# Optimization experiments

Hardware: AMD Instinct MI355X
Metric: run time of the kernel (lower is better)

The kernel has to match this reference:

```python
import jax, jax.numpy as jnp
import numpy as np

N_NODES = 50000
N_EDGES = 500000
D_IN = 128
D_HID = 128
OUTPUT_DIM = 10.0


def gcn_conv(x, src, dst, edge_weight, W, b, n_nodes):
    # PyG GCNConv: out = D^{-1/2} (A + I) D^{-1/2} X W + b, self-loop weight 1
    xw = x @ W  # [N, D_out]
    # degree at target nodes, including self-loop weight 1
    deg = jax.ops.segment_sum(edge_weight, dst, num_segments=n_nodes) + 1.0
    dinv = jnp.where(deg > 0, jax.lax.rsqrt(deg), 0.0)  # [N]
    norm = dinv[src] * edge_weight * dinv[dst]  # [E]
    msgs = xw[src] * norm[:, None]  # [E, D_out] gathered+scaled messages
    agg = jax.ops.segment_sum(msgs, dst, num_segments=n_nodes)
    # analytic self-loop contribution: norm_ii = dinv_i * 1 * dinv_i
    agg = agg + xw * (dinv * dinv)[:, None]
    return agg + b


def setup_inputs() -> dict:
    key = jax.random.key(0)
    k = jax.random.split(key, 8)
    x = jax.random.normal(k[0], (N_NODES, D_IN), dtype=jnp.float32)
    edge_index = jax.random.randint(k[1], (2, N_EDGES), 0, N_NODES, dtype=jnp.int64)
    edge_weight = jax.random.uniform(k[2], (N_EDGES,), dtype=jnp.float32)
    s1 = 1.0 / np.sqrt(D_IN)
    s2 = 1.0 / np.sqrt(D_HID)
    W1 = jax.random.uniform(k[3], (D_IN, D_HID), minval=-s1, maxval=s1, dtype=jnp.float32)
    b1 = jnp.zeros((D_HID,), dtype=jnp.float32)
    W2 = jax.random.uniform(k[4], (D_HID, D_HID), minval=-s2, maxval=s2, dtype=jnp.float32)
    b2 = jnp.zeros((D_HID,), dtype=jnp.float32)
    Wf = jax.random.uniform(k[5], (D_HID, 1), minval=-s2, maxval=s2, dtype=jnp.float32)
    bf = jax.random.uniform(k[6], (1,), minval=-s2, maxval=s2, dtype=jnp.float32)
    return {"x": x, "edge_index": edge_index, "edge_weight": edge_weight,
            "W1": W1, "b1": b1, "W2": W2, "b2": b2, "Wf": Wf, "bf": bf}


def reference(x, edge_index, edge_weight, W1, b1, W2, b2, Wf, bf):
    src, dst = edge_index[0], edge_index[1]
    h = gcn_conv(x, src, dst, edge_weight, W1, b1, N_NODES)
    h = gcn_conv(h, src, dst, edge_weight, W2, b2, N_NODES)
    out = h @ Wf + bf  # [N, 1]
    return jax.nn.sigmoid(out) * OUTPUT_DIM
```

## Files before the change

### kernel.cpp

```cpp
#include <hip/hip_runtime.h>

#define N_NODES 50000
#define N_EDGES 500000
#define D 128
#define CAP 64
#define NCHUNK 256
#define EPC ((N_EDGES + NCHUNK - 1) / NCHUNK)
#define NWORDS ((N_NODES + 3) / 4)

typedef unsigned long long u64;

__global__ void hist_kernel(const int* __restrict__ dst,
                            const float* __restrict__ W1, const float* __restrict__ W2,
                            const float* __restrict__ b1, const float* __restrict__ b2,
                            const float* __restrict__ Wf, const float* __restrict__ bf,
                            unsigned* __restrict__ hist32, float* __restrict__ v,
                            float* __restrict__ consts) {
    if ((int)blockIdx.x == NCHUNK) {
        __shared__ float u[D];
        int t = threadIdx.x;
        if (t < D) {
            float a = 0.f;
#pragma unroll 8
            for (int j = 0; j < D; ++j) a += W2[t * D + j] * Wf[j];
            u[t] = a;
        }
        __syncthreads();
        if (t < D) {
            float a = 0.f;
#pragma unroll 8
            for (int k = 0; k < D; ++k) a += W1[t * D + k] * u[k];
            v[t] = a;
        }
        if (t == 0) {
            float c = 0.f;
            for (int k = 0; k < D; ++k) c += b1[k] * u[k];
            consts[0] = c;
        } else if (t == 1) {
            float c = bf[0];
            for (int k = 0; k < D; ++k) c += b2[k] * Wf[k];
            consts[1] = c;
        }
        return;
    }
    __shared__ unsigned lds[NWORDS];
    const int t = threadIdx.x;
    const int c = blockIdx.x;
    for (int i = t; i < NWORDS; i += 256) lds[i] = 0u;
    __syncthreads();
    const int e0 = c * EPC;
    const int e1 = (e0 + EPC < N_EDGES) ? e0 + EPC : N_EDGES;
    for (int e = e0 + t; e < e1; e += 256) {
        int d = dst[e];
        atomicAdd(&lds[d >> 2], 1u << (8 * (d & 3)));
    }
    __syncthreads();
    unsigned* outw = hist32 + (size_t)c * NWORDS;
    for (int i = t; i < NWORDS; i += 256) outw[i] = lds[i];
}

__global__ void scan_kernel(const unsigned char* __restrict__ hist8,
                            unsigned char* __restrict__ base8, int* __restrict__ cntv) {
    int n = blockIdx.x * blockDim.x + threadIdx.x;
    if (n >= N_NODES) return;
    int run = 0;
#pragma unroll 8
    for (int c = 0; c < NCHUNK; ++c) {
        int b = hist8[(size_t)c * (NWORDS * 4) + n];
        base8[(size_t)c * (NWORDS * 4) + n] = (unsigned char)run;
        run += b;
    }
    cntv[n] = (run < CAP) ? run : CAP;
}

__global__ void place_kernel(const int* __restrict__ src, const int* __restrict__ dst,
                             const float* __restrict__ ew,
                             const unsigned* __restrict__ base32, int2* __restrict__ pairs) {
    __shared__ unsigned lds[NWORDS];
    const int t = threadIdx.x;
    const int c = blockIdx.x;
    const unsigned* inw = base32 + (size_t)c * NWORDS;
    for (int i = t; i < NWORDS; i += 256) lds[i] = inw[i];
    __syncthreads();
    const int e0 = c * EPC;
    const int e1 = (e0 + EPC < N_EDGES) ? e0 + EPC : N_EDGES;
    for (int e = e0 + t; e < e1; e += 256) {
        int d = dst[e];
        int sh = 8 * (d & 3);
        unsigned old = atomicAdd(&lds[d >> 2], 1u << sh);
        int slot = (int)((old >> sh) & 0xffu);
        if (slot < CAP)
            pairs[(size_t)d * CAP + slot] = make_int2(src[e], __float_as_int(ew[e]));
    }
}

__global__ void gemv_kernel(const float* __restrict__ x, const float* __restrict__ v,
                            const int2* __restrict__ pairs, const int* __restrict__ cntv,
                            float* __restrict__ dinv, float* __restrict__ tw) {
    __shared__ float vs[D];
    const int t = threadIdx.x;
    if (t < D) vs[t] = v[t];
    __syncthreads();
    const int l = t & 31;
    const int n = blockIdx.x * 8 + (t >> 5);
    float4 xv = ((const float4*)(x + (size_t)n * D))[l];
    float a = xv.x * vs[l * 4] + xv.y * vs[l * 4 + 1] +
              xv.z * vs[l * 4 + 2] + xv.w * vs[l * 4 + 3];
    int cnt = cntv[n];
    const int2* row = pairs + (size_t)n * CAP;
    float wsum = 0.f;
    for (int i = l; i < cnt; i += 32) wsum += __int_as_float(row[i].y);
#pragma unroll
    for (int off = 16; off > 0; off >>= 1) {
        a    += __shfl_xor(a, off);
        wsum += __shfl_xor(wsum, off);
    }
    if (l == 0) {
        float di = rsqrtf(wsum + 1.0f);
        dinv[n] = di;
        tw[n] = di * a;
    }
}

__global__ void gather_s_kernel(const float* __restrict__ tw, const float* __restrict__ dinv,
                                const int* __restrict__ cntv, const int2* __restrict__ pairs,
                                const float* __restrict__ consts, float* __restrict__ sw) {
    int tid = threadIdx.x;
    int n = blockIdx.x * 64 + (tid >> 2);
    int l = tid & 3;
    if (n >= N_NODES) return;
    int cnt = cntv[n];
    const int4* row = (const int4*)(pairs + (size_t)n * CAP);
    float acc = 0.f;
    for (int c = l; 2 * c < cnt; c += 4) {
        int4 p = row[c];
        acc += __int_as_float(p.y) * tw[p.x];
        if (2 * c + 1 < cnt) acc += __int_as_float(p.w) * tw[p.z];
    }
    acc += __shfl_xor(acc, 1);
    acc += __shfl_xor(acc, 2);
    if (l == 0) {
        float di = dinv[n];
        float s = di * (acc + tw[n]) + consts[0];
        sw[n] = di * s;
    }
}

__global__ void gather_z_kernel(const float* __restrict__ sw, const float* __restrict__ dinv,
                                const int* __restrict__ cntv, const int2* __restrict__ pairs,
                                const float* __restrict__ consts, float* __restrict__ out) {
    int tid = threadIdx.x;
    int n = blockIdx.x * 64 + (tid >> 2);
    int l = tid & 3;
    if (n >= N_NODES) return;
    int cnt = cntv[n];
    const int4* row = (const int4*)(pairs + (size_t)n * CAP);
    float acc = 0.f;
    for (int c = l; 2 * c < cnt; c += 4) {
        int4 p = row[c];
        acc += __int_as_float(p.y) * sw[p.x];
        if (2 * c + 1 < cnt) acc += __int_as_float(p.w) * sw[p.z];
    }
    acc += __shfl_xor(acc, 1);
    acc += __shfl_xor(acc, 2);
    if (l == 0) {
        float di = dinv[n];
        float z = di * (acc + sw[n]) + consts[1];
        out[n] = 10.0f / (1.0f + expf(-z));
    }
}

extern "C" void kernel_launch(void* const* d_in, const int* in_sizes, int n_in,
                              void* d_out, int out_size, void* d_ws, size_t ws_size,
                              hipStream_t stream) {
    const float* x  = (const float*)d_in[0];
    const int*   ei = (const int*)d_in[1];
    const float* ew = (const float*)d_in[2];
    const float* W1 = (const float*)d_in[3];
    const float* b1 = (const float*)d_in[4];
    const float* W2 = (const float*)d_in[5];
    const float* b2 = (const float*)d_in[6];
    const float* Wf = (const float*)d_in[7];
    const float* bf = (const float*)d_in[8];
    const int* srcv = ei;
    const int* dstv = ei + N_EDGES;
    float* out = (float*)d_out;

    char* p = (char*)d_ws;
    auto alloc = [&](size_t bytes) { void* r = (void*)p; p += (bytes + 255) & ~(size_t)255; return r; };
    unsigned*      hist32 = (unsigned*)alloc((size_t)NCHUNK * NWORDS * 4);
    unsigned char* base8  = (unsigned char*)alloc((size_t)NCHUNK * NWORDS * 4);
    int*   cntv   = (int*)alloc(N_NODES * 4);
    float* dinv   = (float*)alloc(N_NODES * 4);
    float* tw     = (float*)alloc(N_NODES * 4);
    float* sw     = (float*)alloc(N_NODES * 4);
    float* v      = (float*)alloc(D * 4);
    float* consts = (float*)alloc(2 * 4);
    int2*  pairs  = (int2*)alloc((size_t)N_NODES * CAP * 8);

    const int GB = (N_NODES + 63) / 64;
    const int NB = (N_NODES + 255) / 256;

    hist_kernel<<<NCHUNK + 1, 256, 0, stream>>>(dstv, W1, W2, b1, b2, Wf, bf,
                                                hist32, v, consts);

    scan_kernel<<<NB, 256, 0, stream>>>((const unsigned char*)hist32, base8, cntv);

    place_kernel<<<NCHUNK, 256, 0, stream>>>(srcv, dstv, ew,
                                             (const unsigned*)base8, pairs);

    gemv_kernel<<<N_NODES / 8, 256, 0, stream>>>(x, v, pairs, cntv, dinv, tw);

    gather_s_kernel<<<GB, 256, 0, stream>>>(tw, dinv, cntv, pairs, consts, sw);
    gather_z_kernel<<<GB, 256, 0, stream>>>(sw, dinv, cntv, pairs, consts, out);
}
```

Measured before the change: 140.8 us.

## Rewrite chunk scan as packed-word LDS scan across chunk partitions

Replaces the per-node serial byte scan over 256 chunks with a block-level scan operating on packed 32-bit words (four byte counters each), splitting the chunk dimension across four thread groups with an LDS carry combine. Reads and writes become 32-bit coalesced instead of byte-wide strided, and cntv is written as int4. Relies on byte counters not overflowing into neighbours, which the original byte layout already assumed. Uses 64KB+ of LDS per block, which limits occupancy.

```diff
diff --git a/kernel.cpp b/kernel.cpp
--- a/kernel.cpp
+++ b/kernel.cpp
@@ -5,10 +5,10 @@
 #define D 128
 #define CAP 64
 #define NCHUNK 256
-#define EPC ((N_EDGES + NCHUNK - 1) / NCHUNK)
-#define NWORDS ((N_NODES + 3) / 4)
-
-typedef unsigned long long u64;
+#define EPC 1954
+#define NWORDS 12500
+#define SCAN_W 64
+#define SCAN_BLOCKS ((NWORDS + SCAN_W - 1) / SCAN_W)
 
 __global__ void hist_kernel(const int* __restrict__ dst,
                             const float* __restrict__ W1, const float* __restrict__ W2,
@@ -59,18 +59,51 @@
     for (int i = t; i < NWORDS; i += 256) outw[i] = lds[i];
 }
 
-__global__ void scan_kernel(const unsigned char* __restrict__ hist8,
-                            unsigned char* __restrict__ base8, int* __restrict__ cntv) {
-    int n = blockIdx.x * blockDim.x + threadIdx.x;
-    if (n >= N_NODES) return;
-    int run = 0;
-#pragma unroll 8
-    for (int c = 0; c < NCHUNK; ++c) {
-        int b = hist8[(size_t)c * (NWORDS * 4) + n];
-        base8[(size_t)c * (NWORDS * 4) + n] = (unsigned char)run;
-        run += b;
-    }
-    cntv[n] = (run < CAP) ? run : CAP;
+__global__ __launch_bounds__(256) void scan_kernel(const unsigned* __restrict__ hist32,
+                                                   unsigned* __restrict__ base32,
+                                                   int* __restrict__ cntv) {
+    __shared__ unsigned lds[NCHUNK][SCAN_W];
+    __shared__ unsigned tot[4][SCAN_W];
+    const int t = threadIdx.x;
+    const int cp = t >> 6;
+    const int w = t & 63;
+    const int gw = blockIdx.x * SCAN_W + w;
+    const bool valid = gw < NWORDS;
+    for (int cc = 0; cc < 64; ++cc) {
+        int c = cp * 64 + cc;
+        lds[c][w] = valid ? hist32[(size_t)c * NWORDS + gw] : 0u;
+    }
+    __syncthreads();
+    unsigned run = 0u;
+    for (int cc = 0; cc < 64; ++cc) {
+        int c = cp * 64 + cc;
+        unsigned x = lds[c][w];
+        lds[c][w] = run;
+        run += x;
+    }
+    tot[cp][w] = run;
+    __syncthreads();
+    unsigned off = 0u;
+    for (int j = 0; j < cp; ++j) off += tot[j][w];
+    for (int cc = 0; cc < 64; ++cc) {
+        int c = cp * 64 + cc;
+        lds[c][w] += off;
+    }
+    if (cp == 0 && valid) {
+        unsigned tl = tot[0][w] + tot[1][w] + tot[2][w] + tot[3][w];
+        int4 cv;
+        cv.x = min((int)(tl & 0xffu), CAP);
+        cv.y = min((int)((tl >> 8) & 0xffu), CAP);
+        cv.z = min((int)((tl >> 16) & 0xffu), CAP);
+        cv.w = min((int)((tl >> 24) & 0xffu), CAP);
+        ((int4*)cntv)[gw] = cv;
+    }
+    if (valid) {
+        for (int cc = 0; cc < 64; ++cc) {
+            int c = cp * 64 + cc;
+            base32[(size_t)c * NWORDS + gw] = lds[c][w];
+        }
+    }
 }
 
 __global__ void place_kernel(const int* __restrict__ src, const int* __restrict__ dst,
@@ -188,8 +221,8 @@
 
     char* p = (char*)d_ws;
     auto alloc = [&](size_t bytes) { void* r = (void*)p; p += (bytes + 255) & ~(size_t)255; return r; };
-    unsigned*      hist32 = (unsigned*)alloc((size_t)NCHUNK * NWORDS * 4);
-    unsigned char* base8  = (unsigned char*)alloc((size_t)NCHUNK * NWORDS * 4);
+    unsigned* hist32 = (unsigned*)alloc((size_t)NCHUNK * NWORDS * 4);
+    unsigned* base32 = (unsigned*)alloc((size_t)NCHUNK * NWORDS * 4);
     int*   cntv   = (int*)alloc(N_NODES * 4);
     float* dinv   = (float*)alloc(N_NODES * 4);
     float* tw     = (float*)alloc(N_NODES * 4);
@@ -199,15 +232,11 @@
     int2*  pairs  = (int2*)alloc((size_t)N_NODES * CAP * 8);
 
     const int GB = (N_NODES + 63) / 64;
-    const int NB = (N_NODES + 255) / 256;
 
     hist_kernel<<<NCHUNK + 1, 256, 0, stream>>>(dstv, W1, W2, b1, b2, Wf, bf,
                                                 hist32, v, consts);
-
-    scan_kernel<<<NB, 256, 0, stream>>>((const unsigned char*)hist32, base8, cntv);
-
-    place_kernel<<<NCHUNK, 256, 0, stream>>>(srcv, dstv, ew,
-                                             (const unsigned*)base8, pairs);
+    scan_kernel<<<SCAN_BLOCKS, 256, 0, stream>>>(hist32, base32, cntv);
+    place_kernel<<<NCHUNK, 256, 0, stream>>>(srcv, dstv, ew, base32, pairs);
 
     gemv_kernel<<<N_NODES / 8, 256, 0, stream>>>(x, v, pairs, cntv, dinv, tw);
 
```

Result: slower. 149.4 us (+6.1%).

## Replace per-chunk byte histograms with two-level bucketed CSR construction

Applied to the files above, without the earlier changes.

Replaces the 256-chunk LDS byte histogram, per-node serial scan and placement into fixed 64-slot rows with a two-pass bucket sort. The first pass scatters edge records into 98 coarse destination buckets through global atomic allocation. The second pass builds a compact CSR per 512-node bucket with an LDS count, a scan and placement, and rows are padded to even length for int4 reads. This removes the large hist/base arrays and the sparse padded pair layout, in exchange for an extra record write and read. Correctness relies on each bucket holding at most 8192 edges, which holds for uniform random inputs.

```diff
diff --git a/kernel.cpp b/kernel.cpp
--- a/kernel.cpp
+++ b/kernel.cpp
@@ -2,100 +2,132 @@
 
 #define N_NODES 50000
 #define N_EDGES 500000
+#define NQ (N_EDGES / 4)
 #define D 128
 #define CAP 64
-#define NCHUNK 256
-#define EPC ((N_EDGES + NCHUNK - 1) / NCHUNK)
-#define NWORDS ((N_NODES + 3) / 4)
-
-typedef unsigned long long u64;
-
-__global__ void hist_kernel(const int* __restrict__ dst,
-                            const float* __restrict__ W1, const float* __restrict__ W2,
+#define NBUCK 98
+#define BN 512
+#define REG 8192
+
+__global__ void prep_kernel(const float* __restrict__ W1, const float* __restrict__ W2,
                             const float* __restrict__ b1, const float* __restrict__ b2,
                             const float* __restrict__ Wf, const float* __restrict__ bf,
-                            unsigned* __restrict__ hist32, float* __restrict__ v,
-                            float* __restrict__ consts) {
-    if ((int)blockIdx.x == NCHUNK) {
-        __shared__ float u[D];
-        int t = threadIdx.x;
-        if (t < D) {
-            float a = 0.f;
+                            float* __restrict__ v, float* __restrict__ consts,
+                            unsigned* __restrict__ alloc) {
+    const int t = threadIdx.x;
+    if (blockIdx.x == 1) {
+        if (t < 128) alloc[t] = 0u;
+        return;
+    }
+    __shared__ float u[D];
+    if (t < D) {
+        float a = 0.f;
 #pragma unroll 8
-            for (int j = 0; j < D; ++j) a += W2[t * D + j] * Wf[j];
-            u[t] = a;
-        }
+        for (int j = 0; j < D; ++j) a += W2[t * D + j] * Wf[j];
+        u[t] = a;
+    }
+    __syncthreads();
+    if (t < D) {
+        float a = 0.f;
+#pragma unroll 8
+        for (int k = 0; k < D; ++k) a += W1[t * D + k] * u[k];
+        v[t] = a;
+    }
+    if (t == 0) {
+        float c = 0.f;
+        for (int k = 0; k < D; ++k) c += b1[k] * u[k];
+        consts[0] = c;
+    } else if (t == 1) {
+        float c = bf[0];
+        for (int k = 0; k < D; ++k) c += b2[k] * Wf[k];
+        consts[1] = c;
+    }
+}
+
+__global__ void bucket_kernel(const int* __restrict__ src, const int* __restrict__ dst,
+                              const float* __restrict__ ew,
+                              unsigned* __restrict__ alloc, unsigned* __restrict__ recs) {
+    __shared__ unsigned hist[NBUCK];
+    const int t = threadIdx.x;
+    if (t < NBUCK) hist[t] = 0u;
+    __syncthreads();
+    const int q = blockIdx.x * 256 + t;
+    const bool act = q < NQ;
+    int4 d4 = make_int4(0, 0, 0, 0), s4 = make_int4(0, 0, 0, 0);
+    float4 w4 = make_float4(0.f, 0.f, 0.f, 0.f);
+    int b0 = 0, b1 = 0, b2 = 0, b3 = 0;
+    if (act) {
+        d4 = ((const int4*)dst)[q];
+        s4 = ((const int4*)src)[q];
+        w4 = ((const float4*)ew)[q];
+        b0 = d4.x >> 9; b1 = d4.y >> 9; b2 = d4.z >> 9; b3 = d4.w >> 9;
+        atomicAdd(&hist[b0], 1u); atomicAdd(&hist[b1], 1u);
+        atomicAdd(&hist[b2], 1u); atomicAdd(&hist[b3], 1u);
+    }
+    __syncthreads();
+    if (t < NBUCK) hist[t] = atomicAdd(&alloc[t], hist[t]);
+    __syncthreads();
+    if (act) {
+        unsigned p;
+        p = atomicAdd(&hist[b0], 1u);
+        if (p < REG) { size_t o = ((size_t)b0 * REG + p) * 3;
+            recs[o] = (unsigned)d4.x; recs[o+1] = (unsigned)s4.x; recs[o+2] = __float_as_uint(w4.x); }
+        p = atomicAdd(&hist[b1], 1u);
+        if (p < REG) { size_t o = ((size_t)b1 * REG + p) * 3;
+            recs[o] = (unsigned)d4.y; recs[o+1] = (unsigned)s4.y; recs[o+2] = __float_as_uint(w4.y); }
+        p = atomicAdd(&hist[b2], 1u);
+        if (p < REG) { size_t o = ((size_t)b2 * REG + p) * 3;
+            recs[o] = (unsigned)d4.z; recs[o+1] = (unsigned)s4.z; recs[o+2] = __float_as_uint(w4.z); }
+        p = atomicAdd(&hist[b3], 1u);
+        if (p < REG) { size_t o = ((size_t)b3 * REG + p) * 3;
+            recs[o] = (unsigned)d4.w; recs[o+1] = (unsigned)s4.w; recs[o+2] = __float_as_uint(w4.w); }
+    }
+}
+
+__global__ __launch_bounds__(512) void csr_kernel(const unsigned* __restrict__ recs,
+                                                  const unsigned* __restrict__ alloc,
+                                                  int2* __restrict__ csr,
+                                                  unsigned* __restrict__ rowptr,
+                                                  int* __restrict__ cntv) {
+    __shared__ unsigned cnt[BN], pfx[BN], cur[BN];
+    const int b = blockIdx.x, t = threadIdx.x;
+    const int nb0 = b * BN;
+    const int nnode = (N_NODES - nb0 < BN) ? (N_NODES - nb0) : BN;
+    unsigned total = alloc[b];
+    if (total > REG) total = REG;
+    cnt[t] = 0u;
+    __syncthreads();
+    const unsigned* rb = recs + (size_t)b * REG * 3;
+    for (unsigned i = t; i < total; i += 512)
+        atomicAdd(&cnt[rb[i * 3] - nb0], 1u);
+    __syncthreads();
+    const unsigned c = cnt[t];
+    const unsigned cR = (c + 1u) & ~1u;
+    pfx[t] = cR;
+    __syncthreads();
+    for (int off = 1; off < BN; off <<= 1) {
+        unsigned vv = (t >= off) ? pfx[t - off] : 0u;
         __syncthreads();
-        if (t < D) {
-            float a = 0.f;
-#pragma unroll 8
-            for (int k = 0; k < D; ++k) a += W1[t * D + k] * u[k];
-            v[t] = a;
-        }
-        if (t == 0) {
-            float c = 0.f;
-            for (int k = 0; k < D; ++k) c += b1[k] * u[k];
-            consts[0] = c;
-        } else if (t == 1) {
-            float c = bf[0];
-            for (int k = 0; k < D; ++k) c += b2[k] * Wf[k];
-            consts[1] = c;
-        }
-        return;
-    }
-    __shared__ unsigned lds[NWORDS];
-    const int t = threadIdx.x;
-    const int c = blockIdx.x;
-    for (int i = t; i < NWORDS; i += 256) lds[i] = 0u;
-    __syncthreads();
-    const int e0 = c * EPC;
-    const int e1 = (e0 + EPC < N_EDGES) ? e0 + EPC : N_EDGES;
-    for (int e = e0 + t; e < e1; e += 256) {
-        int d = dst[e];
-        atomicAdd(&lds[d >> 2], 1u << (8 * (d & 3)));
-    }
-    __syncthreads();
-    unsigned* outw = hist32 + (size_t)c * NWORDS;
-    for (int i = t; i < NWORDS; i += 256) outw[i] = lds[i];
-}
-
-__global__ void scan_kernel(const unsigned char* __restrict__ hist8,
-                            unsigned char* __restrict__ base8, int* __restrict__ cntv) {
-    int n = blockIdx.x * blockDim.x + threadIdx.x;
-    if (n >= N_NODES) return;
-    int run = 0;
-#pragma unroll 8
-    for (int c = 0; c < NCHUNK; ++c) {
-        int b = hist8[(size_t)c * (NWORDS * 4) + n];
-        base8[(size_t)c * (NWORDS * 4) + n] = (unsigned char)run;
-        run += b;
-    }
-    cntv[n] = (run < CAP) ? run : CAP;
-}
-
-__global__ void place_kernel(const int* __restrict__ src, const int* __restrict__ dst,
-                             const float* __restrict__ ew,
-                             const unsigned* __restrict__ base32, int2* __restrict__ pairs) {
-    __shared__ unsigned lds[NWORDS];
-    const int t = threadIdx.x;
-    const int c = blockIdx.x;
-    const unsigned* inw = base32 + (size_t)c * NWORDS;
-    for (int i = t; i < NWORDS; i += 256) lds[i] = inw[i];
-    __syncthreads();
-    const int e0 = c * EPC;
-    const int e1 = (e0 + EPC < N_EDGES) ? e0 + EPC : N_EDGES;
-    for (int e = e0 + t; e < e1; e += 256) {
-        int d = dst[e];
-        int sh = 8 * (d & 3);
-        unsigned old = atomicAdd(&lds[d >> 2], 1u << sh);
-        int slot = (int)((old >> sh) & 0xffu);
-        if (slot < CAP)
-            pairs[(size_t)d * CAP + slot] = make_int2(src[e], __float_as_int(ew[e]));
+        pfx[t] += vv;
+        __syncthreads();
+    }
+    const unsigned excl = pfx[t] - cR;
+    cur[t] = excl;
+    if (t < nnode) {
+        rowptr[nb0 + t] = (unsigned)(b * REG) + excl;
+        cntv[nb0 + t] = (c < CAP) ? (int)c : CAP;
+    }
+    __syncthreads();
+    for (unsigned i = t; i < total; i += 512) {
+        unsigned d = rb[i * 3], s = rb[i * 3 + 1], w = rb[i * 3 + 2];
+        unsigned r = atomicAdd(&cur[d - nb0], 1u);
+        csr[(size_t)b * REG + r] = make_int2((int)s, (int)w);
     }
 }
 
 __global__ void gemv_kernel(const float* __restrict__ x, const float* __restrict__ v,
-                            const int2* __restrict__ pairs, const int* __restrict__ cntv,
+                            const int2* __restrict__ csr, const unsigned* __restrict__ rowptr,
+                            const int* __restrict__ cntv,
                             float* __restrict__ dinv, float* __restrict__ tw) {
     __shared__ float vs[D];
     const int t = threadIdx.x;
@@ -107,7 +139,7 @@
     float a = xv.x * vs[l * 4] + xv.y * vs[l * 4 + 1] +
               xv.z * vs[l * 4 + 2] + xv.w * vs[l * 4 + 3];
     int cnt = cntv[n];
-    const int2* row = pairs + (size_t)n * CAP;
+    const int2* row = csr + rowptr[n];
     float wsum = 0.f;
     for (int i = l; i < cnt; i += 32) wsum += __int_as_float(row[i].y);
 #pragma unroll
@@ -123,14 +155,15 @@
 }
 
 __global__ void gather_s_kernel(const float* __restrict__ tw, const float* __restrict__ dinv,
-                                const int* __restrict__ cntv, const int2* __restrict__ pairs,
+                                const int* __restrict__ cntv, const int2* __restrict__ csr,
+                                const unsigned* __restrict__ rowptr,
                                 const float* __restrict__ consts, float* __restrict__ sw) {
     int tid = threadIdx.x;
     int n = blockIdx.x * 64 + (tid >> 2);
     int l = tid & 3;
     if (n >= N_NODES) return;
     int cnt = cntv[n];
-    const int4* row = (const int4*)(pairs + (size_t)n * CAP);
+    const int4* row = (const int4*)(csr + rowptr[n]);
     float acc = 0.f;
     for (int c = l; 2 * c < cnt; c += 4) {
         int4 p = row[c];
@@ -147,14 +180,15 @@
 }
 
 __global__ void gather_z_kernel(const float* __restrict__ sw, const float* __restrict__ dinv,
-                                const int* __restrict__ cntv, const int2* __restrict__ pairs,
+                                const int* __restrict__ cntv, const int2* __restrict__ csr,
+                                const unsigned* __restrict__ rowptr,
                                 const float* __restrict__ consts, float* __restrict__ out) {
     int tid = threadIdx.x;
     int n = blockIdx.x * 64 + (tid >> 2);
     int l = tid & 3;
     if (n >= N_NODES) return;
     int cnt = cntv[n];
-    const int4* row = (const int4*)(pairs + (size_t)n * CAP);
+    const int4* row = (const int4*)(csr + rowptr[n]);
     float acc = 0.f;
     for (int c = l; 2 * c < cnt; c += 4) {
         int4 p = row[c];
@@ -187,30 +221,28 @@
     float* out = (float*)d_out;
 
     char* p = (char*)d_ws;
-    auto alloc = [&](size_t bytes) { void* r = (void*)p; p += (bytes + 255) & ~(size_t)255; return r; };
-    unsigned*      hist32 = (unsigned*)alloc((size_t)NCHUNK * NWORDS * 4);
-    unsigned char* base8  = (unsigned char*)alloc((size_t)NCHUNK * NWORDS * 4);
-    int*   cntv   = (int*)alloc(N_NODES * 4);
-    float* dinv   = (float*)alloc(N_NODES * 4);
-    float* tw     = (float*)alloc(N_NODES * 4);
-    float* sw     = (float*)alloc(N_NODES * 4);
-    float* v      = (float*)alloc(D * 4);
-    float* consts = (float*)alloc(2 * 4);
-    int2*  pairs  = (int2*)alloc((size_t)N_NODES * CAP * 8);
-
+    auto alloc_ws = [&](size_t bytes) { void* r = (void*)p; p += (bytes + 255) & ~(size_t)255; return r; };
+    unsigned* alloc  = (unsigned*)alloc_ws(128 * 4);
+    unsigned* recs   = (unsigned*)alloc_ws((size_t)NBUCK * REG * 12);
+    int2*     csr    = (int2*)alloc_ws((size_t)NBUCK * REG * 8);
+    unsigned* rowptr = (unsigned*)alloc_ws(N_NODES * 4);
+    int*      cntv   = (int*)alloc_ws(N_NODES * 4);
+    float*    dinv   = (float*)alloc_ws(N_NODES * 4);
+    float*    tw     = (float*)alloc_ws(N_NODES * 4);
+    float*    sw     = (float*)alloc_ws(N_NODES * 4);
+    float*    v      = (float*)alloc_ws(D * 4);
+    float*    consts = (float*)alloc_ws(2 * 4);
+
+    const int AB = (NQ + 255) / 256;
     const int GB = (N_NODES + 63) / 64;
-    const int NB = (N_NODES + 255) / 256;
-
-    hist_kernel<<<NCHUNK + 1, 256, 0, stream>>>(dstv, W1, W2, b1, b2, Wf, bf,
-                                                hist32, v, consts);
-
-    scan_kernel<<<NB, 256, 0, stream>>>((const unsigned char*)hist32, base8, cntv);
-
-    place_kernel<<<NCHUNK, 256, 0, stream>>>(srcv, dstv, ew,
-                                             (const unsigned*)base8, pairs);
-
-    gemv_kernel<<<N_NODES / 8, 256, 0, stream>>>(x, v, pairs, cntv, dinv, tw);
-
-    gather_s_kernel<<<GB, 256, 0, stream>>>(tw, dinv, cntv, pairs, consts, sw);
-    gather_z_kernel<<<GB, 256, 0, stream>>>(sw, dinv, cntv, pairs, consts, out);
-}
+
+    prep_kernel<<<2, 256, 0, stream>>>(W1, W2, b1, b2, Wf, bf, v, consts, alloc);
+
+    bucket_kernel<<<AB, 256, 0, stream>>>(srcv, dstv, ew, alloc, recs);
+    csr_kernel<<<NBUCK, 512, 0, stream>>>(recs, alloc, csr, rowptr, cntv);
+
+    gemv_kernel<<<N_NODES / 8, 256, 0, stream>>>(x, v, csr, rowptr, cntv, dinv, tw);
+
+    gather_s_kernel<<<GB, 256, 0, stream>>>(tw, dinv, cntv, csr, rowptr, consts, sw);
+    gather_z_kernel<<<GB, 256, 0, stream>>>(sw, dinv, cntv, csr, rowptr, consts, out);
+}
```

New measurement: 135.8 us. 1.04x faster.
